# Kernel optimization log

Hardware: AMD Instinct MI355X
Metric: run time of the kernel (lower is better)

Reference implementation:

```python
import jax, jax.numpy as jnp
import numpy as np

B, N, S = 8, 512, 96
SD = TD = H = 256
NH, HD = 8, 32  # num_heads, head_dim
OUT = 4


def setup_inputs() -> dict:
    key = jax.random.key(0)
    ks = jax.random.split(key, 20)
    g = lambda k, shape: (jax.random.normal(k, shape, dtype=jnp.float32) * 0.02)
    return {
        "spatial_features": jax.random.normal(ks[0], (B, N, SD), dtype=jnp.float32),
        "temporal_features": jax.random.normal(ks[1], (B, S, TD), dtype=jnp.float32),
        "Ws": g(ks[2], (H, SD)),   "bs": g(ks[3], (H,)),
        "Wt": g(ks[4], (H, TD)),   "bt": g(ks[5], (H,)),
        "Win": g(ks[6], (3 * H, H)), "bin": g(ks[7], (3 * H,)),
        "Wao": g(ks[8], (H, H)),   "bao": g(ks[9], (H,)),
        "W1": g(ks[10], (H, H)),   "b1": g(ks[11], (H,)),
        "Wo1": g(ks[12], (H // 2, H)), "bo1": g(ks[13], (H // 2,)),
        "Wo2": g(ks[14], (OUT, H // 2)), "bo2": g(ks[15], (OUT,)),
    }


def reference(spatial_features, temporal_features, Ws, bs, Wt, bt, Win, bin, Wao, bao,
              W1, b1, Wo1, bo1, Wo2, bo2):
    # Projections
    sp = spatial_features @ Ws.T + bs          # [B, N, H]
    tp = temporal_features @ Wt.T + bt         # [B, S, H]
    # MultiheadAttention in_proj (batched over all N node-queries at once;
    # mathematically identical to the original per-node loop)
    Wq, Wk, Wv = Win[:H], Win[H:2 * H], Win[2 * H:]
    bq, bk, bv = bin[:H], bin[H:2 * H], bin[2 * H:]
    q = (sp @ Wq.T + bq).reshape(B, N, NH, HD)   # [B, N, h, d]
    k = (tp @ Wk.T + bk).reshape(B, S, NH, HD)   # [B, S, h, d]
    v = (tp @ Wv.T + bv).reshape(B, S, NH, HD)
    scale = 1.0 / np.sqrt(HD).astype(np.float32)
    logits = jnp.einsum('bnhd,bshd->bhns', q * scale, k)   # [B, h, N, S]
    attn = jax.nn.softmax(logits, axis=-1)
    ctx = jnp.einsum('bhns,bshd->bnhd', attn, v).reshape(B, N, H)
    attended = ctx @ Wao.T + bao               # [B, N, H] (out_proj)
    # fusion_layer: Linear + ReLU (dropout=identity in eval)
    fused = jax.nn.relu(attended @ W1.T + b1)  # [B, N, H]
    # output_layer: Linear -> ReLU -> Linear
    h2 = jax.nn.relu(fused @ Wo1.T + bo1)      # [B, N, H/2]
    y = h2 @ Wo2.T + bo2                       # [B, N, OUT]
    # original expands over seq_len BEFORE fusion_layer; since all layers are
    # pointwise over the (S, N) grid, compute once per node and broadcast.
    return jnp.broadcast_to(y[:, None, :, :], (B, S, N, OUT))
```

## Files before the change

kernel.cpp:

```cpp
#include <hip/hip_runtime.h>

#define BB 8
#define NN 512
#define SS 96
#define HH 256
#define NHD 8
#define HDD 32
#define OUTD 4

#define WSB_OFF  0
#define WQB_OFF  65536
#define WAOB_OFF 131072
#define W1B_OFF  196608
#define WO1B_OFF 262144
#define CAST_TOTAL 294912
#define KB_OFF   294912
#define VTB_OFF  491520

typedef __attribute__((ext_vector_type(8))) short bf16x8;
typedef __attribute__((ext_vector_type(4))) float f32x4;

__device__ __forceinline__ unsigned short f2bf(float f) {
    unsigned int u = __float_as_uint(f);
    u = (u + 0x7FFFu + ((u >> 16) & 1u)) >> 16;
    return (unsigned short)u;
}

__device__ __forceinline__ bf16x8 ldw8(const float* __restrict__ p) {
    float4 a = *(const float4*)p, b = *(const float4*)(p + 4);
    bf16x8 r;
    r[0] = (short)f2bf(a.x); r[1] = (short)f2bf(a.y);
    r[2] = (short)f2bf(a.z); r[3] = (short)f2bf(a.w);
    r[4] = (short)f2bf(b.x); r[5] = (short)f2bf(b.y);
    r[6] = (short)f2bf(b.z); r[7] = (short)f2bf(b.w);
    return r;
}

template<int NCT>
__device__ __forceinline__ void mfma_stage(
    const unsigned short* __restrict__ Asw,
    const unsigned short* __restrict__ Wb,
    int lane, int wave, f32x4 acc[NCT])
{
    const int row = lane & 15, kq = lane >> 4;
    #pragma unroll
    for (int ct = 0; ct < NCT; ++ct) acc[ct] = (f32x4){0.f, 0.f, 0.f, 0.f};
    #pragma unroll 2
    for (int kt = 0; kt < 8; ++kt) {
        const int slot = kt * 4 + kq;
        bf16x8 a = *(const bf16x8*)(Asw + row * 256 + ((slot ^ (row & 7)) << 3));
        #pragma unroll
        for (int ct = 0; ct < NCT; ++ct) {
            const unsigned short* wp =
                Wb + (size_t)((wave * NCT + ct) * 16 + row) * 256 + kt * 32 + kq * 8;
            bf16x8 b = *(const bf16x8*)wp;
            acc[ct] = __builtin_amdgcn_mfma_f32_16x16x32_bf16(a, b, acc[ct], 0, 0, 0);
        }
    }
}

template<int NCT>
__device__ __forceinline__ void mfma_stage_f32w(
    const unsigned short* __restrict__ Asw,
    const float* __restrict__ Wf,
    int lane, int wave, f32x4 acc[NCT])
{
    const int row = lane & 15, kq = lane >> 4;
    #pragma unroll
    for (int ct = 0; ct < NCT; ++ct) acc[ct] = (f32x4){0.f, 0.f, 0.f, 0.f};
    #pragma unroll 2
    for (int kt = 0; kt < 8; ++kt) {
        const int slot = kt * 4 + kq;
        bf16x8 a = *(const bf16x8*)(Asw + row * 256 + ((slot ^ (row & 7)) << 3));
        #pragma unroll
        for (int ct = 0; ct < NCT; ++ct) {
            const float* wp =
                Wf + (size_t)((wave * NCT + ct) * 16 + row) * 256 + kt * 32 + kq * 8;
            bf16x8 b = ldw8(wp);
            acc[ct] = __builtin_amdgcn_mfma_f32_16x16x32_bf16(a, b, acc[ct], 0, 0, 0);
        }
    }
}

template<int NCT, bool RELU>
__device__ __forceinline__ void epi_lds(
    unsigned short* __restrict__ OutSw, const float* __restrict__ bias,
    int lane, int wave, const f32x4 acc[NCT])
{
    const int col0 = lane & 15, rq = lane >> 4;
    #pragma unroll
    for (int ct = 0; ct < NCT; ++ct) {
        const int C = wave * NCT * 16 + ct * 16 + col0;
        const float bb = bias[C];
        const int slot = C >> 3, within = C & 7;
        #pragma unroll
        for (int r = 0; r < 4; ++r) {
            const int R = rq * 4 + r;
            float v = acc[ct][r] + bb;
            if (RELU) v = fmaxf(v, 0.f);
            OutSw[R * 256 + ((slot ^ (R & 7)) << 3) + within] = f2bf(v);
        }
    }
}

template<int NCT>
__device__ __forceinline__ void epi_gbf16(
    unsigned short* __restrict__ Og, const float* __restrict__ bias,
    int lane, int wave, const f32x4 acc[NCT])
{
    const int col0 = lane & 15, rq = lane >> 4;
    #pragma unroll
    for (int ct = 0; ct < NCT; ++ct) {
        const int C = wave * NCT * 16 + ct * 16 + col0;
        const float bb = bias[C];
        #pragma unroll
        for (int r = 0; r < 4; ++r) {
            const int R = rq * 4 + r;
            Og[(size_t)R * 256 + C] = f2bf(acc[ct][r] + bb);
        }
    }
}

template<int NT>
__device__ __forceinline__ void stage_A(
    const float* __restrict__ Ag, unsigned short* __restrict__ Asw, int tid)
{
    #pragma unroll
    for (int ii = 0; ii < 1024 / NT; ++ii) {
        int i = tid + ii * NT;
        int row = i >> 6, c4 = i & 63;
        float4 v = ((const float4*)(Ag + (size_t)row * 256))[c4];
        int col = c4 * 4;
        int slot = col >> 3, half = (col >> 2) & 1;
        ushort4 o;
        o.x = f2bf(v.x); o.y = f2bf(v.y); o.z = f2bf(v.z); o.w = f2bf(v.w);
        *(ushort4*)(Asw + row * 256 + ((slot ^ (row & 7)) << 3) + half * 4) = o;
    }
}

__global__ __launch_bounds__(512) void k_prep(
    const float* __restrict__ temporal,
    const float* __restrict__ bt, const float* __restrict__ bin,
    const float* __restrict__ Wt, const float* __restrict__ Win,
    const float* __restrict__ Ws, const float* __restrict__ Wao,
    const float* __restrict__ W1, const float* __restrict__ Wo1,
    unsigned short* __restrict__ kb, unsigned short* __restrict__ vtb,
    unsigned short* __restrict__ bfw)
{
    const int tid = threadIdx.x;
    if (blockIdx.x < 192) {
        __shared__ __align__(16) unsigned short A0[16 * 256];
        __shared__ __align__(16) unsigned short MID[16 * 256];
        const int lane = tid & 63, wave = tid >> 6;
        const int m = blockIdx.x >> 2;
        const int c = blockIdx.x & 3;
        const int r0 = m * 16;
        f32x4 acc[2];
        stage_A<512>(temporal + (size_t)r0 * 256, A0, tid);
        __syncthreads();
        mfma_stage_f32w<2>(A0, Wt, lane, wave, acc);
        epi_lds<2, false>(MID, bt, lane, wave, acc);
        __syncthreads();
        f32x4 a1[1];
        if (c < 2) {
            mfma_stage_f32w<1>(MID, Win + (size_t)(256 + c * 128) * 256, lane, wave, a1);
            epi_gbf16<1>(kb + (size_t)r0 * 256 + c * 128, bin + 256 + c * 128,
                         lane, wave, a1);
        } else {
            mfma_stage_f32w<1>(MID, Win + (size_t)(512 + (c - 2) * 128) * 256, lane, wave, a1);
            const int bb_ = r0 / 96, s0 = r0 % 96;
            const int col0 = lane & 15, rq = lane >> 4;
            const int Cl = (c - 2) * 128 + wave * 16 + col0;
            const float bv = bin[512 + Cl];
            #pragma unroll
            for (int r = 0; r < 4; ++r) {
                const int R = rq * 4 + r;
                vtb[((size_t)(bb_ * 256 + Cl)) * 96 + s0 + R] = f2bf(a1[0][r] + bv);
            }
        }
    } else {
        int idx = (blockIdx.x - 192) * 512 + tid;
        for (int j4 = idx; j4 < CAST_TOTAL / 4; j4 += 24 * 512) {
            int e = j4 * 4;
            const float* src; int off;
            if (e < 65536)       { src = Ws;  off = e; }
            else if (e < 131072) { src = Win; off = e - 65536; }
            else if (e < 196608) { src = Wao; off = e - 131072; }
            else if (e < 262144) { src = W1;  off = e - 196608; }
            else                 { src = Wo1; off = e - 262144; }
            float4 v = *(const float4*)(src + off);
            ushort4 o;
            o.x = f2bf(v.x); o.y = f2bf(v.y); o.z = f2bf(v.z); o.w = f2bf(v.w);
            *(ushort4*)(bfw + e) = o;
        }
    }
}

__global__ __launch_bounds__(512) void k_main(
    const float* __restrict__ spatial,
    const float* __restrict__ bs, const float* __restrict__ bin,
    const unsigned short* __restrict__ bfw,
    const unsigned short* __restrict__ kb, const unsigned short* __restrict__ vtb,
    const float* __restrict__ bao, const float* __restrict__ b1,
    const float* __restrict__ bo1,
    const float* __restrict__ Wo2, const float* __restrict__ bo2,
    float* __restrict__ out)
{
    __shared__ __align__(16) unsigned short A0[16 * 256];
    __shared__ __align__(16) unsigned short MID[16 * 256];
    __shared__ __align__(16) unsigned short Q[16 * 256];
    __shared__ __align__(16) unsigned short P[8][16 * 104];
    __shared__ __align__(16) float H2[16 * 128];
    __shared__ __align__(16) float y[16][OUTD];
    const int tid = threadIdx.x, lane = tid & 63, wave = tid >> 6;
    const int b = blockIdx.x >> 5;
    const int n0 = (blockIdx.x & 31) * 16;
    const int cl = lane & 15, kq = lane >> 4;
    const float scale = 0.17677669529663687f;
    f32x4 acc[2];

    stage_A<512>(spatial + (size_t)(b * NN + n0) * 256, A0, tid);
    __syncthreads();
    mfma_stage<2>(A0, bfw + WSB_OFF, lane, wave, acc);
    epi_lds<2, false>(MID, bs, lane, wave, acc);
    __syncthreads();
    mfma_stage<2>(MID, bfw + WQB_OFF, lane, wave, acc);
    epi_lds<2, false>(Q, bin, lane, wave, acc);

    unsigned short* Pw = &P[wave][0];
    {
        const int h = wave;
        const int slotq = h * 4 + kq;
        bf16x8 aq = *(const bf16x8*)(Q + cl * 256 + ((slotq ^ (cl & 7)) << 3));
        f32x4 l[6];
        #pragma unroll
        for (int t = 0; t < 6; ++t) {
            bf16x8 bk = *(const bf16x8*)(kb + (size_t)(b * SS + t * 16 + cl) * 256 + h * 32 + kq * 8);
            l[t] = __builtin_amdgcn_mfma_f32_16x16x32_bf16(aq, bk, (f32x4){0.f,0.f,0.f,0.f}, 0, 0, 0);
        }
        float pr[6][4];
        float sum[4] = {0.f, 0.f, 0.f, 0.f};
        #pragma unroll
        for (int t = 0; t < 6; ++t)
            #pragma unroll
            for (int r = 0; r < 4; ++r) {
                float p = __expf(l[t][r] * scale);
                pr[t][r] = p; sum[r] += p;
            }
        #pragma unroll
        for (int r = 0; r < 4; ++r) {
            float s = sum[r];
            s += __shfl_xor(s, 1); s += __shfl_xor(s, 2);
            s += __shfl_xor(s, 4); s += __shfl_xor(s, 8);
            sum[r] = 1.0f / s;
        }
        #pragma unroll
        for (int t = 0; t < 6; ++t)
            #pragma unroll
            for (int r = 0; r < 4; ++r)
                Pw[(kq * 4 + r) * 104 + t * 16 + cl] = f2bf(pr[t][r] * sum[r]);
        f32x4 c0 = (f32x4){0.f,0.f,0.f,0.f}, c1 = (f32x4){0.f,0.f,0.f,0.f};
        #pragma unroll
        for (int ks = 0; ks < 3; ++ks) {
            bf16x8 pa = *(const bf16x8*)(Pw + cl * 104 + ks * 32 + kq * 8);
            bf16x8 v0 = *(const bf16x8*)(vtb + (size_t)(b * 256 + h * 32 + cl) * 96 + ks * 32 + kq * 8);
            bf16x8 v1 = *(const bf16x8*)(vtb + (size_t)(b * 256 + h * 32 + 16 + cl) * 96 + ks * 32 + kq * 8);
            c0 = __builtin_amdgcn_mfma_f32_16x16x32_bf16(pa, v0, c0, 0, 0, 0);
            c1 = __builtin_amdgcn_mfma_f32_16x16x32_bf16(pa, v1, c1, 0, 0, 0);
        }
        #pragma unroll
        for (int dt = 0; dt < 2; ++dt) {
            const f32x4 cc = dt ? c1 : c0;
            const int C = h * 32 + dt * 16 + cl;
            const int slot = C >> 3, within = C & 7;
            #pragma unroll
            for (int r = 0; r < 4; ++r) {
                const int R = kq * 4 + r;
                A0[R * 256 + ((slot ^ (R & 7)) << 3) + within] = f2bf(cc[r]);
            }
        }
    }
    __syncthreads();

    mfma_stage<2>(A0, bfw + WAOB_OFF, lane, wave, acc);
    epi_lds<2, false>(MID, bao, lane, wave, acc);
    __syncthreads();
    mfma_stage<2>(MID, bfw + W1B_OFF, lane, wave, acc);
    epi_lds<2, true>(A0, b1, lane, wave, acc);
    __syncthreads();
    {
        f32x4 a1[1];
        mfma_stage<1>(A0, bfw + WO1B_OFF, lane, wave, a1);
        const int rq = lane >> 4;
        const int C = wave * 16 + cl;
        const float bb = bo1[C];
        #pragma unroll
        for (int r = 0; r < 4; ++r) {
            const int R = rq * 4 + r;
            H2[R * 128 + C] = fmaxf(a1[0][r] + bb, 0.f);
        }
    }
    __syncthreads();
    if (tid < 64) {
        int r = tid >> 2, o = tid & 3;
        float a = 0.f;
        const float4* w4 = (const float4*)(Wo2 + (size_t)o * 128);
        const float4* h4 = (const float4*)(H2 + r * 128);
        for (int kk = 0; kk < 32; ++kk) {
            float4 w = w4[kk], hv = h4[kk];
            a += hv.x * w.x + hv.y * w.y + hv.z * w.z + hv.w * w.w;
        }
        y[r][o] = a + bo2[o];
    }
    __syncthreads();
    for (int i = tid; i < 16 * SS; i += 512) {
        int s = i >> 4;
        int r = i & 15;
        *(float4*)(out + ((size_t)(b * SS + s) * NN + (n0 + r)) * OUTD) = *(const float4*)y[r];
    }
}

extern "C" void kernel_launch(void* const* d_in, const int* in_sizes, int n_in,
                              void* d_out, int out_size, void* d_ws, size_t ws_size,
                              hipStream_t stream) {
    const float* spatial  = (const float*)d_in[0];
    const float* temporal = (const float*)d_in[1];
    const float* Ws  = (const float*)d_in[2];
    const float* bs  = (const float*)d_in[3];
    const float* Wt  = (const float*)d_in[4];
    const float* bt  = (const float*)d_in[5];
    const float* Win = (const float*)d_in[6];
    const float* bin = (const float*)d_in[7];
    const float* Wao = (const float*)d_in[8];
    const float* bao = (const float*)d_in[9];
    const float* W1  = (const float*)d_in[10];
    const float* b1  = (const float*)d_in[11];
    const float* Wo1 = (const float*)d_in[12];
    const float* bo1 = (const float*)d_in[13];
    const float* Wo2 = (const float*)d_in[14];
    const float* bo2 = (const float*)d_in[15];
    float* out = (float*)d_out;
    unsigned short* wsu = (unsigned short*)d_ws;

    unsigned short* bfw = wsu;
    unsigned short* kb  = wsu + KB_OFF;
    unsigned short* vtb = wsu + VTB_OFF;

    hipLaunchKernelGGL(k_prep, dim3(216), dim3(512), 0, stream,
                       temporal, bt, bin, Wt, Win, Ws, Wao, W1, Wo1,
                       kb, vtb, bfw);
    hipLaunchKernelGGL(k_main, dim3(256), dim3(512), 0, stream,
                       spatial, bs, bin, bfw, kb, vtb,
                       bao, b1, bo1, Wo2, bo2, out);
}
```

Before: 123.3 us.

## Fuse prep and main kernels into one cooperative launch with grid sync

Merges the K/V projection and weight-cast prep kernel with the main attention/MLP kernel into a single cooperative kernel of 256 blocks, separated by a grid-wide barrier. Blocks 192-255 now do the weight casting with a wider stride. The aim is to remove the second kernel launch and the gap between kernels. In exchange, every block must wait at a grid barrier, and occupancy is limited by launch_bounds(512,2), which cooperative launch requires for co-residency.

```diff
diff --git a/kernel.cpp b/kernel.cpp
--- a/kernel.cpp
+++ b/kernel.cpp
@@ -1,4 +1,7 @@
 #include <hip/hip_runtime.h>
+#include <hip/hip_cooperative_groups.h>
+
+namespace cg = cooperative_groups;
 
 #define BB 8
 #define NN 512
@@ -138,20 +141,28 @@
     }
 }
 
-__global__ __launch_bounds__(512) void k_prep(
-    const float* __restrict__ temporal,
-    const float* __restrict__ bt, const float* __restrict__ bin,
-    const float* __restrict__ Wt, const float* __restrict__ Win,
-    const float* __restrict__ Ws, const float* __restrict__ Wao,
-    const float* __restrict__ W1, const float* __restrict__ Wo1,
+__global__ __launch_bounds__(512, 2) void k_fused(
+    const float* __restrict__ spatial, const float* __restrict__ temporal,
+    const float* __restrict__ Ws, const float* __restrict__ bs,
+    const float* __restrict__ Wt, const float* __restrict__ bt,
+    const float* __restrict__ Win, const float* __restrict__ bin,
+    const float* __restrict__ Wao, const float* __restrict__ bao,
+    const float* __restrict__ W1, const float* __restrict__ b1,
+    const float* __restrict__ Wo1, const float* __restrict__ bo1,
+    const float* __restrict__ Wo2, const float* __restrict__ bo2,
     unsigned short* __restrict__ kb, unsigned short* __restrict__ vtb,
-    unsigned short* __restrict__ bfw)
-{
-    const int tid = threadIdx.x;
+    unsigned short* __restrict__ bfw, float* __restrict__ out)
+{
+    __shared__ __align__(16) unsigned short A0[16 * 256];
+    __shared__ __align__(16) unsigned short MID[16 * 256];
+    __shared__ __align__(16) unsigned short Q[16 * 256];
+    __shared__ __align__(16) unsigned short P[8][16 * 104];
+    __shared__ __align__(16) float H2[16 * 128];
+    __shared__ __align__(16) float y[16][OUTD];
+    const int tid = threadIdx.x, lane = tid & 63, wave = tid >> 6;
+    const int cl = lane & 15, kq = lane >> 4;
+
     if (blockIdx.x < 192) {
-        __shared__ __align__(16) unsigned short A0[16 * 256];
-        __shared__ __align__(16) unsigned short MID[16 * 256];
-        const int lane = tid & 63, wave = tid >> 6;
         const int m = blockIdx.x >> 2;
         const int c = blockIdx.x & 3;
         const int r0 = m * 16;
@@ -169,8 +180,8 @@
         } else {
             mfma_stage_f32w<1>(MID, Win + (size_t)(512 + (c - 2) * 128) * 256, lane, wave, a1);
             const int bb_ = r0 / 96, s0 = r0 % 96;
-            const int col0 = lane & 15, rq = lane >> 4;
-            const int Cl = (c - 2) * 128 + wave * 16 + col0;
+            const int rq = lane >> 4;
+            const int Cl = (c - 2) * 128 + wave * 16 + cl;
             const float bv = bin[512 + Cl];
             #pragma unroll
             for (int r = 0; r < 4; ++r) {
@@ -180,7 +191,7 @@
         }
     } else {
         int idx = (blockIdx.x - 192) * 512 + tid;
-        for (int j4 = idx; j4 < CAST_TOTAL / 4; j4 += 24 * 512) {
+        for (int j4 = idx; j4 < CAST_TOTAL / 4; j4 += 64 * 512) {
             int e = j4 * 4;
             const float* src; int off;
             if (e < 65536)       { src = Ws;  off = e; }
@@ -194,28 +205,11 @@
             *(ushort4*)(bfw + e) = o;
         }
     }
-}
-
-__global__ __launch_bounds__(512) void k_main(
-    const float* __restrict__ spatial,
-    const float* __restrict__ bs, const float* __restrict__ bin,
-    const unsigned short* __restrict__ bfw,
-    const unsigned short* __restrict__ kb, const unsigned short* __restrict__ vtb,
-    const float* __restrict__ bao, const float* __restrict__ b1,
-    const float* __restrict__ bo1,
-    const float* __restrict__ Wo2, const float* __restrict__ bo2,
-    float* __restrict__ out)
-{
-    __shared__ __align__(16) unsigned short A0[16 * 256];
-    __shared__ __align__(16) unsigned short MID[16 * 256];
-    __shared__ __align__(16) unsigned short Q[16 * 256];
-    __shared__ __align__(16) unsigned short P[8][16 * 104];
-    __shared__ __align__(16) float H2[16 * 128];
-    __shared__ __align__(16) float y[16][OUTD];
-    const int tid = threadIdx.x, lane = tid & 63, wave = tid >> 6;
+
+    cg::this_grid().sync();
+
     const int b = blockIdx.x >> 5;
     const int n0 = (blockIdx.x & 31) * 16;
-    const int cl = lane & 15, kq = lane >> 4;
     const float scale = 0.17677669529663687f;
     f32x4 acc[2];
 
@@ -346,10 +340,14 @@
     unsigned short* kb  = wsu + KB_OFF;
     unsigned short* vtb = wsu + VTB_OFF;
 
-    hipLaunchKernelGGL(k_prep, dim3(216), dim3(512), 0, stream,
-                       temporal, bt, bin, Wt, Win, Ws, Wao, W1, Wo1,
-                       kb, vtb, bfw);
-    hipLaunchKernelGGL(k_main, dim3(256), dim3(512), 0, stream,
-                       spatial, bs, bin, bfw, kb, vtb,
-                       bao, b1, bo1, Wo2, bo2, out);
-}
+    void* args[] = {
+        (void*)&spatial, (void*)&temporal,
+        (void*)&Ws, (void*)&bs, (void*)&Wt, (void*)&bt,
+        (void*)&Win, (void*)&bin, (void*)&Wao, (void*)&bao,
+        (void*)&W1, (void*)&b1, (void*)&Wo1, (void*)&bo1,
+        (void*)&Wo2, (void*)&bo2,
+        (void*)&kb, (void*)&vtb, (void*)&bfw, (void*)&out
+    };
+    hipLaunchCooperativeKernel((const void*)k_fused, dim3(256), dim3(512),
+                               args, 0, stream);
+}
```

Result: slower. 181.5 us (+47.1%).
